# Optimization experiments

Measured on AMD Instinct MI355X. Metric: run time of the kernel, lower is better.

The kernel has to match this reference:

```python
import jax, jax.numpy as jnp
import numpy as np

NUM_EMBEDDINGS = 1024
EMBEDDING_SIZE = 256


def setup_inputs() -> dict:
    key = jax.random.key(0)
    k1, k2 = jax.random.split(key)
    z_e = jax.random.normal(k1, (32, 32, 32, EMBEDDING_SIZE), dtype=jnp.float32)
    # original init: uniform(-limit, limit), limit = sqrt(3/num_embeddings)
    limit = np.sqrt(3.0 / NUM_EMBEDDINGS)
    embeddings = jax.random.uniform(
        k2, (NUM_EMBEDDINGS, EMBEDDING_SIZE), dtype=jnp.float32,
        minval=-limit, maxval=limit)
    return {"z_e": z_e, "embeddings": embeddings}


def reference(z_e, embeddings):
    D = embeddings.shape[1]
    z_e_flat = z_e.reshape(-1, D)  # [N, D]
    distances = (
        jnp.sum(z_e_flat * z_e_flat, axis=1, keepdims=True)
        - 2.0 * (z_e_flat @ embeddings.T)
        + jnp.sum(embeddings * embeddings, axis=1)[None, :]
    )  # [N, K]
    z = jnp.argmin(distances, axis=-1).reshape(z_e.shape[:-1])  # indices
    z_q = embeddings[z]  # gather -> same shape as z_e
    return z, z_q
```

## Files before the change

kernel.cpp:

```cpp
#include <hip/hip_runtime.h>
#include <math.h>

#define N_ROWS 32768
#define DIM 256
#define K_CODES 1024
#define MARGIN 2e-3f

typedef float f32x4v __attribute__((ext_vector_type(4)));
typedef short s16x8 __attribute__((ext_vector_type(8)));

#define WS_NEEDED ((size_t)1183748)

__device__ __forceinline__ unsigned short bf16_rne(float f) {
    unsigned int u = __float_as_uint(f);
    unsigned int r = (u + 0x7FFFu + ((u >> 16) & 1u)) >> 16;
    return (unsigned short)r;
}
__device__ __forceinline__ float bf16_f32(unsigned short h) {
    return __uint_as_float(((unsigned int)h) << 16);
}

__device__ __forceinline__ float np_block128_sumsq(const float* e) {
#pragma clang fp contract(off)
    float s[16];
#pragma unroll
    for (int l = 0; l < 16; ++l) {
        float a0 = e[l]       * e[l];
        float a1 = e[16 + l]  * e[16 + l];
        float a2 = e[32 + l]  * e[32 + l];
        float a3 = e[48 + l]  * e[48 + l];
        float a4 = e[64 + l]  * e[64 + l];
        float a5 = e[80 + l]  * e[80 + l];
        float a6 = e[96 + l]  * e[96 + l];
        float a7 = e[112 + l] * e[112 + l];
        s[l] = ((a0 + a1) + (a2 + a3)) + ((a4 + a5) + (a6 + a7));
    }
    float t1[8];
#pragma unroll
    for (int i = 0; i < 8; ++i) t1[i] = s[i] + s[i + 8];
    float t2[4];
#pragma unroll
    for (int i = 0; i < 4; ++i) t2[i] = t1[i] + t1[i + 4];
    return (t2[0] + t2[2]) + (t2[1] + t2[3]);
}

__global__ __launch_bounds__(64) void npsumsq_kernel(const float* __restrict__ src,
                                                     float* __restrict__ dst) {
    __shared__ float buf[16][257];
    const int tid = threadIdx.x;
    const int r0 = blockIdx.x * 16;
#pragma unroll
    for (int it = 0; it < 16; ++it) {
        int idx = it * 64 + tid;
        int r = idx >> 6, c4 = idx & 63;
        float4 v = ((const float4*)(src + (size_t)(r0 + r) * DIM))[c4];
        buf[r][c4 * 4 + 0] = v.x;
        buf[r][c4 * 4 + 1] = v.y;
        buf[r][c4 * 4 + 2] = v.z;
        buf[r][c4 * 4 + 3] = v.w;
    }
    __syncthreads();
    if (tid < 16) {
        const float* e = buf[tid];
        dst[r0 + tid] = np_block128_sumsq(e) + np_block128_sumsq(e + 128);
    }
}

__global__ void zero_kernel(int* p) { if (threadIdx.x == 0) p[0] = 0; }

__global__ __launch_bounds__(64) void wprep_kernel(const float* __restrict__ w,
                                                   float* __restrict__ w2,
                                                   unsigned short* __restrict__ wfrag) {
    __shared__ float buf[16][257];
    const int lane = threadIdx.x;
    const int t = blockIdx.x;
    const int r0 = t * 16;
#pragma unroll
    for (int it = 0; it < 16; ++it) {
        int idx = it * 64 + lane;
        int r = idx >> 6, c4 = idx & 63;
        float4 v = ((const float4*)(w + (size_t)(r0 + r) * DIM))[c4];
        buf[r][c4 * 4 + 0] = v.x;
        buf[r][c4 * 4 + 1] = v.y;
        buf[r][c4 * 4 + 2] = v.z;
        buf[r][c4 * 4 + 3] = v.w;
    }
    __syncthreads();
    if (lane < 16) {
        const float* e = buf[lane];
        w2[r0 + lane] = np_block128_sumsq(e) + np_block128_sumsq(e + 128);
    }
    const int c = lane & 15, ko = lane >> 4;
#pragma unroll
    for (int q = 0; q < 8; ++q) {
        s16x8 hh, ll;
#pragma unroll
        for (int i = 0; i < 8; ++i) {
            float f = buf[c][q * 32 + ko * 8 + i];
            unsigned short h = bf16_rne(f);
            hh[i] = (short)h;
            ll[i] = (short)bf16_rne(f - bf16_f32(h));
        }
        unsigned short* dh = wfrag + (size_t)t * 8192 + q * 512 + lane * 8;
        *(s16x8*)dh = hh;
        *(s16x8*)(dh + 4096) = ll;
    }
}

__global__ __launch_bounds__(256, 1) void vq_mfma(
    const float* __restrict__ x, const uint4* __restrict__ wfrag4,
    const float* __restrict__ w2g, const float* __restrict__ w,
    float* __restrict__ zout, float* __restrict__ zq,
    int* __restrict__ flagcnt, int* __restrict__ flaglist) {
    __shared__ uint4 tiles[2][1024];
    __shared__ float sw2[K_CODES];
    __shared__ int widx_s[128];

    const int tid = threadIdx.x;
    const int wave = tid >> 6;
    const int lane = tid & 63;
    const int rowblk = blockIdx.x * 128;
    const int rowbase = rowblk + wave * 32;

    for (int i = tid; i < K_CODES; i += 256) sw2[i] = w2g[i];

    s16x8 ahi0[8], alo0[8], ahi1[8], alo1[8];
    {
        const float* xr0 = x + (size_t)(rowbase + (lane & 15)) * DIM + (lane >> 4) * 8;
        const float* xr1 = xr0 + 16 * DIM;
#pragma unroll
        for (int q = 0; q < 8; ++q) {
            float4 a = *(const float4*)(xr0 + q * 32);
            float4 b = *(const float4*)(xr0 + q * 32 + 4);
            float e0[8] = {a.x, a.y, a.z, a.w, b.x, b.y, b.z, b.w};
            float4 c = *(const float4*)(xr1 + q * 32);
            float4 d = *(const float4*)(xr1 + q * 32 + 4);
            float e1[8] = {c.x, c.y, c.z, c.w, d.x, d.y, d.z, d.w};
#pragma unroll
            for (int i = 0; i < 8; ++i) {
                unsigned short h0 = bf16_rne(e0[i]);
                ahi0[q][i] = (short)h0;
                alo0[q][i] = (short)bf16_rne(e0[i] - bf16_f32(h0));
                unsigned short h1 = bf16_rne(e1[i]);
                ahi1[q][i] = (short)h1;
                alo1[q][i] = (short)bf16_rne(e1[i] - bf16_f32(h1));
            }
        }
    }

#pragma unroll
    for (int s = 0; s < 4; ++s) {
        int idx = wave * 256 + s * 64 + lane;
        tiles[0][idx] = wfrag4[idx];
    }

    float b1[2][4], b2[2][4];
    int i1[2][4];
#pragma unroll
    for (int rf = 0; rf < 2; ++rf)
#pragma unroll
        for (int j = 0; j < 4; ++j) { b1[rf][j] = INFINITY; b2[rf][j] = INFINITY; i1[rf][j] = 0; }

    __syncthreads();

    int cur = 0;
    for (int ct = 0; ct < 64; ++ct) {
        uint4 pf0, pf1, pf2, pf3;
        if (ct < 63) {
            const uint4* g = wfrag4 + (size_t)(ct + 1) * 1024 + wave * 256 + lane;
            pf0 = g[0]; pf1 = g[64]; pf2 = g[128]; pf3 = g[192];
        }
        const uint4* th = tiles[cur];
        f32x4v a0hh = {0.f, 0.f, 0.f, 0.f};
        f32x4v a0hl = {0.f, 0.f, 0.f, 0.f};
        f32x4v a0lh = {0.f, 0.f, 0.f, 0.f};
        f32x4v a1hh = {0.f, 0.f, 0.f, 0.f};
        f32x4v a1hl = {0.f, 0.f, 0.f, 0.f};
        f32x4v a1lh = {0.f, 0.f, 0.f, 0.f};
#pragma unroll
        for (int q = 0; q < 8; ++q) {
            s16x8 Bh = *(const s16x8*)&th[q * 64 + lane];
            s16x8 Bl = *(const s16x8*)&th[512 + q * 64 + lane];
            a0hh = __builtin_amdgcn_mfma_f32_16x16x32_bf16(ahi0[q], Bh, a0hh, 0, 0, 0);
            a0hl = __builtin_amdgcn_mfma_f32_16x16x32_bf16(ahi0[q], Bl, a0hl, 0, 0, 0);
            a0lh = __builtin_amdgcn_mfma_f32_16x16x32_bf16(alo0[q], Bh, a0lh, 0, 0, 0);
            a1hh = __builtin_amdgcn_mfma_f32_16x16x32_bf16(ahi1[q], Bh, a1hh, 0, 0, 0);
            a1hl = __builtin_amdgcn_mfma_f32_16x16x32_bf16(ahi1[q], Bl, a1hl, 0, 0, 0);
            a1lh = __builtin_amdgcn_mfma_f32_16x16x32_bf16(alo1[q], Bh, a1lh, 0, 0, 0);
        }
        const int code = ct * 16 + (lane & 15);
        const float w2v = sw2[code];
#pragma unroll
        for (int j = 0; j < 4; ++j) {
            float d0 = (a0hh[j] + a0hl[j]) + a0lh[j];
            float s0 = w2v - 2.0f * d0;
            if (s0 < b2[0][j]) {
                if (s0 < b1[0][j]) { b2[0][j] = b1[0][j]; b1[0][j] = s0; i1[0][j] = code; }
                else b2[0][j] = s0;
            }
            float d1 = (a1hh[j] + a1hl[j]) + a1lh[j];
            float s1 = w2v - 2.0f * d1;
            if (s1 < b2[1][j]) {
                if (s1 < b1[1][j]) { b2[1][j] = b1[1][j]; b1[1][j] = s1; i1[1][j] = code; }
                else b2[1][j] = s1;
            }
        }
        if (ct < 63) {
            uint4* d = &tiles[cur ^ 1][wave * 256 + lane];
            d[0] = pf0; d[64] = pf1; d[128] = pf2; d[192] = pf3;
            cur ^= 1;
        }
        __syncthreads();
    }

#pragma unroll
    for (int m = 1; m < 16; m <<= 1) {
#pragma unroll
        for (int rf = 0; rf < 2; ++rf)
#pragma unroll
            for (int j = 0; j < 4; ++j) {
                float ov1 = __shfl_xor(b1[rf][j], m);
                int oi = __shfl_xor(i1[rf][j], m);
                float ov2 = __shfl_xor(b2[rf][j], m);
                float nb2 = fminf(fmaxf(b1[rf][j], ov1), fminf(b2[rf][j], ov2));
                if (ov1 < b1[rf][j] || (ov1 == b1[rf][j] && oi < i1[rf][j])) {
                    b1[rf][j] = ov1; i1[rf][j] = oi;
                }
                b2[rf][j] = nb2;
            }
    }
    if ((lane & 15) == 0) {
#pragma unroll
        for (int rf = 0; rf < 2; ++rf)
#pragma unroll
            for (int j = 0; j < 4; ++j) {
                int rl = wave * 32 + rf * 16 + (lane >> 4) * 4 + j;
                int gi = i1[rf][j];
                widx_s[rl] = gi;
                zout[rowblk + rl] = (float)gi;
                if (b2[rf][j] - b1[rf][j] < MARGIN) {
                    int slot = atomicAdd(flagcnt, 1);
                    flaglist[slot] = rowblk + rl;
                }
            }
    }
    __syncthreads();

    const float4* w4 = (const float4*)w;
    float4* zq4 = (float4*)zq;
#pragma unroll
    for (int p = 0; p < 32; ++p) {
        int lin = p * 256 + tid;
        int row = lin >> 6, qq = lin & 63;
        zq4[(size_t)(rowblk + row) * 64 + qq] = w4[(size_t)widx_s[row] * 64 + qq];
    }
}

__global__ __launch_bounds__(256) void rescue_kernel(
    const float* __restrict__ x, const float* __restrict__ w,
    const float* __restrict__ w2g, const int* __restrict__ flagcnt,
    const int* __restrict__ flaglist, float* __restrict__ zout,
    float* __restrict__ zq) {
    __shared__ __align__(16) float xs[DIM];
    __shared__ float dv[256];
    __shared__ int di[256];
    __shared__ int mi_s;
    __shared__ float x2_s;
    const int tid = threadIdx.x;
    const int cnt = flagcnt[0];
    for (int f = blockIdx.x; f < cnt; f += gridDim.x) {
        const int r = flaglist[f];
        __syncthreads();
        for (int i = tid; i < DIM; i += 256) xs[i] = x[(size_t)r * DIM + i];
        __syncthreads();
        if (tid == 0)
            x2_s = np_block128_sumsq(xs) + np_block128_sumsq(xs + 128);
        __syncthreads();
        const float x2vv = x2_s;
        const float4* xs4 = (const float4*)xs;
        const float4* wr0 = (const float4*)(w + (size_t)(tid + 0 * 256) * DIM);
        const float4* wr1 = (const float4*)(w + (size_t)(tid + 1 * 256) * DIM);
        const float4* wr2 = (const float4*)(w + (size_t)(tid + 2 * 256) * DIM);
        const float4* wr3 = (const float4*)(w + (size_t)(tid + 3 * 256) * DIM);
        float acc0 = 0.f, acc1 = 0.f, acc2 = 0.f, acc3 = 0.f;
#pragma unroll 4
        for (int k4 = 0; k4 < DIM / 4; ++k4) {
            float4 xv = xs4[k4];
            float4 w0 = wr0[k4], w1 = wr1[k4], w2 = wr2[k4], w3 = wr3[k4];
            acc0 = __builtin_fmaf(xv.x, w0.x, acc0);
            acc0 = __builtin_fmaf(xv.y, w0.y, acc0);
            acc0 = __builtin_fmaf(xv.z, w0.z, acc0);
            acc0 = __builtin_fmaf(xv.w, w0.w, acc0);
            acc1 = __builtin_fmaf(xv.x, w1.x, acc1);
            acc1 = __builtin_fmaf(xv.y, w1.y, acc1);
            acc1 = __builtin_fmaf(xv.z, w1.z, acc1);
            acc1 = __builtin_fmaf(xv.w, w1.w, acc1);
            acc2 = __builtin_fmaf(xv.x, w2.x, acc2);
            acc2 = __builtin_fmaf(xv.y, w2.y, acc2);
            acc2 = __builtin_fmaf(xv.z, w2.z, acc2);
            acc2 = __builtin_fmaf(xv.w, w2.w, acc2);
            acc3 = __builtin_fmaf(xv.x, w3.x, acc3);
            acc3 = __builtin_fmaf(xv.y, w3.y, acc3);
            acc3 = __builtin_fmaf(xv.z, w3.z, acc3);
            acc3 = __builtin_fmaf(xv.w, w3.w, acc3);
        }
        float bv = INFINITY;
        int bi = 0;
        float accs[4] = {acc0, acc1, acc2, acc3};
#pragma unroll
        for (int cc = 0; cc < 4; ++cc) {
            int c = tid + cc * 256;
            float s = (x2vv - 2.0f * accs[cc]) + w2g[c];
            if (s < bv) { bv = s; bi = c; }
        }
        dv[tid] = bv;
        di[tid] = bi;
        __syncthreads();
        if (tid == 0) {
            float mv = dv[0];
            int mi = di[0];
            for (int t = 1; t < 256; ++t)
                if (dv[t] < mv || (dv[t] == mv && di[t] < mi)) { mv = dv[t]; mi = di[t]; }
            zout[r] = (float)mi;
            mi_s = mi;
        }
        __syncthreads();
        zq[(size_t)r * DIM + tid] = w[(size_t)mi_s * DIM + tid];
    }
}

#define BM 64
#define BN 128
#define BK 64
#define LDX 68

__global__ __launch_bounds__(256) void vq_kernel_lds(
    const float* __restrict__ x, const float* __restrict__ w,
    const float* __restrict__ x2g, const float* __restrict__ w2g,
    float* __restrict__ zout, float* __restrict__ zq) {
    __shared__ float xs[BM * LDX];
    __shared__ float ws_[BN * LDX];
    __shared__ float sw2[K_CODES];
    __shared__ float sx2[BM];
    __shared__ int widx[BM];

    const int tid = threadIdx.x;
    const int bm0 = blockIdx.x * BM;
    const int rg = tid & 15;
    const int cg = tid >> 4;

    for (int i = tid; i < K_CODES; i += 256) sw2[i] = w2g[i];
    if (tid < BM) sx2[tid] = x2g[bm0 + tid];

    float best[4];
    int bidx[4];
#pragma unroll
    for (int i = 0; i < 4; ++i) { best[i] = INFINITY; bidx[i] = 0; }

    const float4* x4 = (const float4*)x;
    const float4* w4 = (const float4*)w;

    for (int cn = 0; cn < K_CODES / BN; ++cn) {
        float acc[4][8];
#pragma unroll
        for (int i = 0; i < 4; ++i)
#pragma unroll
            for (int j = 0; j < 8; ++j) acc[i][j] = 0.f;

        for (int dk = 0; dk < DIM / BK; ++dk) {
            __syncthreads();
#pragma unroll
            for (int p = 0; p < 4; ++p) {
                int l = p * 256 + tid;
                int row = l >> 4, c4 = l & 15;
                float4 v = x4[(size_t)(bm0 + row) * (DIM / 4) + dk * (BK / 4) + c4];
                *(float4*)&xs[row * LDX + c4 * 4] = v;
            }
#pragma unroll
            for (int p = 0; p < 8; ++p) {
                int l = p * 256 + tid;
                int row = l >> 4, c4 = l & 15;
                float4 v = w4[(size_t)(cn * BN + row) * (DIM / 4) + dk * (BK / 4) + c4];
                *(float4*)&ws_[row * LDX + c4 * 4] = v;
            }
            __syncthreads();
#pragma unroll
            for (int d = 0; d < BK; d += 4) {
                float4 xv[4], wv[8];
#pragma unroll
                for (int i = 0; i < 4; ++i)
                    xv[i] = *(const float4*)&xs[(rg + 16 * i) * LDX + d];
#pragma unroll
                for (int j = 0; j < 8; ++j)
                    wv[j] = *(const float4*)&ws_[(cg + 16 * j) * LDX + d];
#pragma unroll
                for (int i = 0; i < 4; ++i)
#pragma unroll
                    for (int j = 0; j < 8; ++j) {
                        acc[i][j] = __builtin_fmaf(xv[i].x, wv[j].x, acc[i][j]);
                        acc[i][j] = __builtin_fmaf(xv[i].y, wv[j].y, acc[i][j]);
                        acc[i][j] = __builtin_fmaf(xv[i].z, wv[j].z, acc[i][j]);
                        acc[i][j] = __builtin_fmaf(xv[i].w, wv[j].w, acc[i][j]);
                    }
            }
        }
#pragma unroll
        for (int j = 0; j < 8; ++j) {
            int c = cn * BN + cg + 16 * j;
            float w2v = sw2[c];
#pragma unroll
            for (int i = 0; i < 4; ++i) {
                float t = sx2[rg + 16 * i] - 2.0f * acc[i][j];
                float s = t + w2v;
                if (s < best[i]) { best[i] = s; bidx[i] = c; }
            }
        }
    }

    __syncthreads();
    float* sval = xs;
    int* sidx = (int*)(xs + 64 * 17);
#pragma unroll
    for (int i = 0; i < 4; ++i) {
        sval[(rg + 16 * i) * 17 + cg] = best[i];
        sidx[(rg + 16 * i) * 17 + cg] = bidx[i];
    }
    __syncthreads();
    if (tid < BM) {
        float bv = INFINITY;
        int bi = 0;
        for (int c = 0; c < 16; ++c) {
            float v = sval[tid * 17 + c];
            int id = sidx[tid * 17 + c];
            if (v < bv || (v == bv && id < bi)) { bv = v; bi = id; }
        }
        widx[tid] = bi;
        zout[bm0 + tid] = (float)bi;
    }
    __syncthreads();
    float4* zq4 = (float4*)zq;
#pragma unroll
    for (int p = 0; p < 16; ++p) {
        int lin = p * 256 + tid;
        int row = lin >> 6, q = lin & 63;
        zq4[(size_t)(bm0 + row) * 64 + q] = w4[(size_t)widx[row] * 64 + q];
    }
}

extern "C" void kernel_launch(void* const* d_in, const int* in_sizes, int n_in,
                              void* d_out, int out_size, void* d_ws, size_t ws_size,
                              hipStream_t stream) {
    const float* z_e = (const float*)d_in[0];
    const float* emb = (const float*)d_in[1];
    float* x2g = (float*)d_ws;
    int* flaglist = (int*)d_ws;
    float* w2g = x2g + N_ROWS;
    unsigned short* wfrag = (unsigned short*)(w2g + K_CODES);
    int* flagcnt = (int*)(wfrag + (size_t)2 * K_CODES * DIM);
    float* zout = (float*)d_out;
    float* zq = (float*)d_out + N_ROWS;

    if (ws_size >= WS_NEEDED) {
        zero_kernel<<<1, 64, 0, stream>>>(flagcnt);
        wprep_kernel<<<K_CODES / 16, 64, 0, stream>>>(emb, w2g, wfrag);
        vq_mfma<<<N_ROWS / 128, 256, 0, stream>>>(z_e, (const uint4*)wfrag, w2g,
                                                  emb, zout, zq, flagcnt, flaglist);
        rescue_kernel<<<256, 256, 0, stream>>>(z_e, emb, w2g, flagcnt,
                                               flaglist, zout, zq);
    } else {
        npsumsq_kernel<<<N_ROWS / 16, 64, 0, stream>>>(z_e, x2g);
        npsumsq_kernel<<<K_CODES / 16, 64, 0, stream>>>(emb, w2g);
        vq_kernel_lds<<<N_ROWS / BM, 256, 0, stream>>>(z_e, emb, x2g, w2g, zout, zq);
    }
}
```

Measured before the change: 150.6 us.

## Split VQ MFMA block into eight waves of 16 rows each

Each 128-row block now runs 512 threads (8 waves) with 16 rows per wave, where it used to run 4 waves with 32 rows each. Every wave holds half as many A fragments and accumulators, and tile loading and the gather are spread over twice as many threads. The goal is more wave-level parallelism per CU to hide LDS and MFMA latency. The cost is that B-tile reads from LDS are amortised over fewer rows per wave, so LDS traffic per MFMA doubles.

```diff
diff --git a/kernel.cpp b/kernel.cpp
--- a/kernel.cpp
+++ b/kernel.cpp
@@ -107,7 +107,7 @@
     }
 }
 
-__global__ __launch_bounds__(256, 1) void vq_mfma(
+__global__ __launch_bounds__(512, 1) void vq_mfma(
     const float* __restrict__ x, const uint4* __restrict__ wfrag4,
     const float* __restrict__ w2g, const float* __restrict__ w,
     float* __restrict__ zout, float* __restrict__ zq,
@@ -120,94 +120,72 @@
     const int wave = tid >> 6;
     const int lane = tid & 63;
     const int rowblk = blockIdx.x * 128;
-    const int rowbase = rowblk + wave * 32;
-
-    for (int i = tid; i < K_CODES; i += 256) sw2[i] = w2g[i];
-
-    s16x8 ahi0[8], alo0[8], ahi1[8], alo1[8];
+    const int rowbase = rowblk + wave * 16;
+
+    for (int i = tid; i < K_CODES; i += 512) sw2[i] = w2g[i];
+
+    s16x8 ahi[8], alo[8];
     {
-        const float* xr0 = x + (size_t)(rowbase + (lane & 15)) * DIM + (lane >> 4) * 8;
-        const float* xr1 = xr0 + 16 * DIM;
+        const float* xr = x + (size_t)(rowbase + (lane & 15)) * DIM + (lane >> 4) * 8;
 #pragma unroll
         for (int q = 0; q < 8; ++q) {
-            float4 a = *(const float4*)(xr0 + q * 32);
-            float4 b = *(const float4*)(xr0 + q * 32 + 4);
-            float e0[8] = {a.x, a.y, a.z, a.w, b.x, b.y, b.z, b.w};
-            float4 c = *(const float4*)(xr1 + q * 32);
-            float4 d = *(const float4*)(xr1 + q * 32 + 4);
-            float e1[8] = {c.x, c.y, c.z, c.w, d.x, d.y, d.z, d.w};
+            float4 a = *(const float4*)(xr + q * 32);
+            float4 b = *(const float4*)(xr + q * 32 + 4);
+            float e[8] = {a.x, a.y, a.z, a.w, b.x, b.y, b.z, b.w};
 #pragma unroll
             for (int i = 0; i < 8; ++i) {
-                unsigned short h0 = bf16_rne(e0[i]);
-                ahi0[q][i] = (short)h0;
-                alo0[q][i] = (short)bf16_rne(e0[i] - bf16_f32(h0));
-                unsigned short h1 = bf16_rne(e1[i]);
-                ahi1[q][i] = (short)h1;
-                alo1[q][i] = (short)bf16_rne(e1[i] - bf16_f32(h1));
-            }
-        }
-    }
-
-#pragma unroll
-    for (int s = 0; s < 4; ++s) {
-        int idx = wave * 256 + s * 64 + lane;
-        tiles[0][idx] = wfrag4[idx];
-    }
-
-    float b1[2][4], b2[2][4];
-    int i1[2][4];
-#pragma unroll
-    for (int rf = 0; rf < 2; ++rf)
-#pragma unroll
-        for (int j = 0; j < 4; ++j) { b1[rf][j] = INFINITY; b2[rf][j] = INFINITY; i1[rf][j] = 0; }
+                unsigned short h = bf16_rne(e[i]);
+                ahi[q][i] = (short)h;
+                alo[q][i] = (short)bf16_rne(e[i] - bf16_f32(h));
+            }
+        }
+    }
+
+    tiles[0][tid] = wfrag4[tid];
+    tiles[0][tid + 512] = wfrag4[tid + 512];
+
+    float b1[4], b2[4];
+    int i1[4];
+#pragma unroll
+    for (int j = 0; j < 4; ++j) { b1[j] = INFINITY; b2[j] = INFINITY; i1[j] = 0; }
 
     __syncthreads();
 
     int cur = 0;
     for (int ct = 0; ct < 64; ++ct) {
-        uint4 pf0, pf1, pf2, pf3;
+        uint4 pf0, pf1;
         if (ct < 63) {
-            const uint4* g = wfrag4 + (size_t)(ct + 1) * 1024 + wave * 256 + lane;
-            pf0 = g[0]; pf1 = g[64]; pf2 = g[128]; pf3 = g[192];
+            const uint4* g = wfrag4 + (size_t)(ct + 1) * 1024;
+            pf0 = g[tid];
+            pf1 = g[tid + 512];
         }
         const uint4* th = tiles[cur];
-        f32x4v a0hh = {0.f, 0.f, 0.f, 0.f};
-        f32x4v a0hl = {0.f, 0.f, 0.f, 0.f};
-        f32x4v a0lh = {0.f, 0.f, 0.f, 0.f};
-        f32x4v a1hh = {0.f, 0.f, 0.f, 0.f};
-        f32x4v a1hl = {0.f, 0.f, 0.f, 0.f};
-        f32x4v a1lh = {0.f, 0.f, 0.f, 0.f};
+        f32x4v ahh = {0.f, 0.f, 0.f, 0.f};
+        f32x4v ahl = {0.f, 0.f, 0.f, 0.f};
+        f32x4v alh = {0.f, 0.f, 0.f, 0.f};
 #pragma unroll
         for (int q = 0; q < 8; ++q) {
             s16x8 Bh = *(const s16x8*)&th[q * 64 + lane];
             s16x8 Bl = *(const s16x8*)&th[512 + q * 64 + lane];
-            a0hh = __builtin_amdgcn_mfma_f32_16x16x32_bf16(ahi0[q], Bh, a0hh, 0, 0, 0);
-            a0hl = __builtin_amdgcn_mfma_f32_16x16x32_bf16(ahi0[q], Bl, a0hl, 0, 0, 0);
-            a0lh = __builtin_amdgcn_mfma_f32_16x16x32_bf16(alo0[q], Bh, a0lh, 0, 0, 0);
-            a1hh = __builtin_amdgcn_mfma_f32_16x16x32_bf16(ahi1[q], Bh, a1hh, 0, 0, 0);
-            a1hl = __builtin_amdgcn_mfma_f32_16x16x32_bf16(ahi1[q], Bl, a1hl, 0, 0, 0);
-            a1lh = __builtin_amdgcn_mfma_f32_16x16x32_bf16(alo1[q], Bh, a1lh, 0, 0, 0);
+            ahh = __builtin_amdgcn_mfma_f32_16x16x32_bf16(ahi[q], Bh, ahh, 0, 0, 0);
+            ahl = __builtin_amdgcn_mfma_f32_16x16x32_bf16(ahi[q], Bl, ahl, 0, 0, 0);
+            alh = __builtin_amdgcn_mfma_f32_16x16x32_bf16(alo[q], Bh, alh, 0, 0, 0);
         }
         const int code = ct * 16 + (lane & 15);
         const float w2v = sw2[code];
 #pragma unroll
         for (int j = 0; j < 4; ++j) {
-            float d0 = (a0hh[j] + a0hl[j]) + a0lh[j];
-            float s0 = w2v - 2.0f * d0;
-            if (s0 < b2[0][j]) {
-                if (s0 < b1[0][j]) { b2[0][j] = b1[0][j]; b1[0][j] = s0; i1[0][j] = code; }
-                else b2[0][j] = s0;
-            }
-            float d1 = (a1hh[j] + a1hl[j]) + a1lh[j];
-            float s1 = w2v - 2.0f * d1;
-            if (s1 < b2[1][j]) {
-                if (s1 < b1[1][j]) { b2[1][j] = b1[1][j]; b1[1][j] = s1; i1[1][j] = code; }
-                else b2[1][j] = s1;
+            float d = (ahh[j] + ahl[j]) + alh[j];
+            float s = w2v - 2.0f * d;
+            if (s < b2[j]) {
+                if (s < b1[j]) { b2[j] = b1[j]; b1[j] = s; i1[j] = code; }
+                else b2[j] = s;
             }
         }
         if (ct < 63) {
-            uint4* d = &tiles[cur ^ 1][wave * 256 + lane];
-            d[0] = pf0; d[64] = pf1; d[128] = pf2; d[192] = pf3;
+            uint4* d = tiles[cur ^ 1];
+            d[tid] = pf0;
+            d[tid + 512] = pf1;
             cur ^= 1;
         }
         __syncthreads();
@@ -216,41 +194,34 @@
 #pragma unroll
     for (int m = 1; m < 16; m <<= 1) {
 #pragma unroll
-        for (int rf = 0; rf < 2; ++rf)
-#pragma unroll
-            for (int j = 0; j < 4; ++j) {
-                float ov1 = __shfl_xor(b1[rf][j], m);
-                int oi = __shfl_xor(i1[rf][j], m);
-                float ov2 = __shfl_xor(b2[rf][j], m);
-                float nb2 = fminf(fmaxf(b1[rf][j], ov1), fminf(b2[rf][j], ov2));
-                if (ov1 < b1[rf][j] || (ov1 == b1[rf][j] && oi < i1[rf][j])) {
-                    b1[rf][j] = ov1; i1[rf][j] = oi;
-                }
-                b2[rf][j] = nb2;
-            }
+        for (int j = 0; j < 4; ++j) {
+            float ov1 = __shfl_xor(b1[j], m);
+            int oi = __shfl_xor(i1[j], m);
+            float ov2 = __shfl_xor(b2[j], m);
+            float nb2 = fminf(fmaxf(b1[j], ov1), fminf(b2[j], ov2));
+            if (ov1 < b1[j] || (ov1 == b1[j] && oi < i1[j])) { b1[j] = ov1; i1[j] = oi; }
+            b2[j] = nb2;
+        }
     }
     if ((lane & 15) == 0) {
 #pragma unroll
-        for (int rf = 0; rf < 2; ++rf)
-#pragma unroll
-            for (int j = 0; j < 4; ++j) {
-                int rl = wave * 32 + rf * 16 + (lane >> 4) * 4 + j;
-                int gi = i1[rf][j];
-                widx_s[rl] = gi;
-                zout[rowblk + rl] = (float)gi;
-                if (b2[rf][j] - b1[rf][j] < MARGIN) {
-                    int slot = atomicAdd(flagcnt, 1);
-                    flaglist[slot] = rowblk + rl;
-                }
-            }
+        for (int j = 0; j < 4; ++j) {
+            int rl = wave * 16 + (lane >> 4) * 4 + j;
+            widx_s[rl] = i1[j];
+            zout[rowblk + rl] = (float)i1[j];
+            if (b2[j] - b1[j] < MARGIN) {
+                int slot = atomicAdd(flagcnt, 1);
+                flaglist[slot] = rowblk + rl;
+            }
+        }
     }
     __syncthreads();
 
     const float4* w4 = (const float4*)w;
     float4* zq4 = (float4*)zq;
 #pragma unroll
-    for (int p = 0; p < 32; ++p) {
-        int lin = p * 256 + tid;
+    for (int p = 0; p < 16; ++p) {
+        int lin = p * 512 + tid;
         int row = lin >> 6, qq = lin & 63;
         zq4[(size_t)(rowblk + row) * 64 + qq] = w4[(size_t)widx_s[row] * 64 + qq];
     }
@@ -463,7 +434,7 @@
     if (ws_size >= WS_NEEDED) {
         zero_kernel<<<1, 64, 0, stream>>>(flagcnt);
         wprep_kernel<<<K_CODES / 16, 64, 0, stream>>>(emb, w2g, wfrag);
-        vq_mfma<<<N_ROWS / 128, 256, 0, stream>>>(z_e, (const uint4*)wfrag, w2g,
+        vq_mfma<<<N_ROWS / 128, 512, 0, stream>>>(z_e, (const uint4*)wfrag, w2g,
                                                   emb, zout, zq, flagcnt, flaglist);
         rescue_kernel<<<256, 256, 0, stream>>>(z_e, emb, w2g, flagcnt,
                                                flaglist, zout, zq);
```

New measurement: 136.1 us. -9.6%, faster.

## Split codebook scan across two wave groups per block and drop zero kernel

Applied to the files above, without the earlier changes.

The MFMA kernel now runs 512 threads per block. Two groups of four waves each scan alternating 16-code tiles for the same 128 rows, and their top-2 results are merged through shared memory at the end. This halves the serial loop length per wave and raises occupancy to two blocks per CU. The cost is duplicated A-fragment registers and a larger LDS tile buffer. The separate zero_kernel launch is folded into wprep_kernel to save one launch.

```diff
diff --git a/kernel.cpp b/kernel.cpp
--- a/kernel.cpp
+++ b/kernel.cpp
@@ -66,15 +66,15 @@
     }
 }
 
-__global__ void zero_kernel(int* p) { if (threadIdx.x == 0) p[0] = 0; }
-
 __global__ __launch_bounds__(64) void wprep_kernel(const float* __restrict__ w,
                                                    float* __restrict__ w2,
-                                                   unsigned short* __restrict__ wfrag) {
+                                                   unsigned short* __restrict__ wfrag,
+                                                   int* __restrict__ flagcnt) {
     __shared__ float buf[16][257];
     const int lane = threadIdx.x;
     const int t = blockIdx.x;
     const int r0 = t * 16;
+    if (t == 0 && lane == 0) flagcnt[0] = 0;
 #pragma unroll
     for (int it = 0; it < 16; ++it) {
         int idx = it * 64 + lane;
@@ -107,22 +107,26 @@
     }
 }
 
-__global__ __launch_bounds__(256, 1) void vq_mfma(
+__global__ __launch_bounds__(512, 2) void vq_mfma(
     const float* __restrict__ x, const uint4* __restrict__ wfrag4,
     const float* __restrict__ w2g, const float* __restrict__ w,
     float* __restrict__ zout, float* __restrict__ zq,
     int* __restrict__ flagcnt, int* __restrict__ flaglist) {
-    __shared__ uint4 tiles[2][1024];
+    __shared__ uint4 tiles[2][2048];
     __shared__ float sw2[K_CODES];
+    __shared__ float M1[128], M2[128];
+    __shared__ int MI[128];
     __shared__ int widx_s[128];
 
     const int tid = threadIdx.x;
     const int wave = tid >> 6;
     const int lane = tid & 63;
+    const int wg = wave >> 2;
+    const int wsub = wave & 3;
     const int rowblk = blockIdx.x * 128;
-    const int rowbase = rowblk + wave * 32;
-
-    for (int i = tid; i < K_CODES; i += 256) sw2[i] = w2g[i];
+    const int rowbase = rowblk + wsub * 32;
+
+    for (int i = tid; i < K_CODES; i += 512) sw2[i] = w2g[i];
 
     s16x8 ahi0[8], alo0[8], ahi1[8], alo1[8];
     {
@@ -148,11 +152,10 @@
         }
     }
 
-#pragma unroll
-    for (int s = 0; s < 4; ++s) {
-        int idx = wave * 256 + s * 64 + lane;
-        tiles[0][idx] = wfrag4[idx];
-    }
+    tiles[0][tid] = wfrag4[tid];
+    tiles[0][tid + 512] = wfrag4[tid + 512];
+    tiles[0][tid + 1024] = wfrag4[tid + 1024];
+    tiles[0][tid + 1536] = wfrag4[tid + 1536];
 
     float b1[2][4], b2[2][4];
     int i1[2][4];
@@ -164,13 +167,14 @@
     __syncthreads();
 
     int cur = 0;
-    for (int ct = 0; ct < 64; ++ct) {
+    for (int p = 0; p < 32; ++p) {
         uint4 pf0, pf1, pf2, pf3;
-        if (ct < 63) {
-            const uint4* g = wfrag4 + (size_t)(ct + 1) * 1024 + wave * 256 + lane;
-            pf0 = g[0]; pf1 = g[64]; pf2 = g[128]; pf3 = g[192];
-        }
-        const uint4* th = tiles[cur];
+        if (p < 31) {
+            const uint4* g = wfrag4 + (size_t)(2 * p + 2) * 1024;
+            pf0 = g[tid]; pf1 = g[tid + 512];
+            pf2 = g[tid + 1024]; pf3 = g[tid + 1536];
+        }
+        const uint4* th = &tiles[cur][wg * 1024];
         f32x4v a0hh = {0.f, 0.f, 0.f, 0.f};
         f32x4v a0hl = {0.f, 0.f, 0.f, 0.f};
         f32x4v a0lh = {0.f, 0.f, 0.f, 0.f};
@@ -188,7 +192,7 @@
             a1hl = __builtin_amdgcn_mfma_f32_16x16x32_bf16(ahi1[q], Bl, a1hl, 0, 0, 0);
             a1lh = __builtin_amdgcn_mfma_f32_16x16x32_bf16(alo1[q], Bh, a1lh, 0, 0, 0);
         }
-        const int code = ct * 16 + (lane & 15);
+        const int code = (2 * p + wg) * 16 + (lane & 15);
         const float w2v = sw2[code];
 #pragma unroll
         for (int j = 0; j < 4; ++j) {
@@ -205,9 +209,10 @@
                 else b2[1][j] = s1;
             }
         }
-        if (ct < 63) {
-            uint4* d = &tiles[cur ^ 1][wave * 256 + lane];
-            d[0] = pf0; d[64] = pf1; d[128] = pf2; d[192] = pf3;
+        if (p < 31) {
+            uint4* d = tiles[cur ^ 1];
+            d[tid] = pf0; d[tid + 512] = pf1;
+            d[tid + 1024] = pf2; d[tid + 1536] = pf3;
             cur ^= 1;
         }
         __syncthreads();
@@ -229,16 +234,36 @@
                 b2[rf][j] = nb2;
             }
     }
-    if ((lane & 15) == 0) {
+    if (wg == 1 && (lane & 15) == 0) {
 #pragma unroll
         for (int rf = 0; rf < 2; ++rf)
 #pragma unroll
             for (int j = 0; j < 4; ++j) {
-                int rl = wave * 32 + rf * 16 + (lane >> 4) * 4 + j;
-                int gi = i1[rf][j];
+                int rl = wsub * 32 + rf * 16 + (lane >> 4) * 4 + j;
+                M1[rl] = b1[rf][j];
+                M2[rl] = b2[rf][j];
+                MI[rl] = i1[rf][j];
+            }
+    }
+    __syncthreads();
+    if (wg == 0 && (lane & 15) == 0) {
+#pragma unroll
+        for (int rf = 0; rf < 2; ++rf)
+#pragma unroll
+            for (int j = 0; j < 4; ++j) {
+                int rl = wsub * 32 + rf * 16 + (lane >> 4) * 4 + j;
+                float a1 = b1[rf][j], a2 = b2[rf][j];
+                int ai = i1[rf][j];
+                float o1 = M1[rl], o2 = M2[rl];
+                int oi = MI[rl];
+                float g1;
+                int gi;
+                if (o1 < a1 || (o1 == a1 && oi < ai)) { g1 = o1; gi = oi; }
+                else { g1 = a1; gi = ai; }
+                float g2 = fminf(fmaxf(a1, o1), fminf(a2, o2));
                 widx_s[rl] = gi;
                 zout[rowblk + rl] = (float)gi;
-                if (b2[rf][j] - b1[rf][j] < MARGIN) {
+                if (g2 - g1 < MARGIN) {
                     int slot = atomicAdd(flagcnt, 1);
                     flaglist[slot] = rowblk + rl;
                 }
@@ -249,8 +274,8 @@
     const float4* w4 = (const float4*)w;
     float4* zq4 = (float4*)zq;
 #pragma unroll
-    for (int p = 0; p < 32; ++p) {
-        int lin = p * 256 + tid;
+    for (int p2 = 0; p2 < 16; ++p2) {
+        int lin = p2 * 512 + tid;
         int row = lin >> 6, qq = lin & 63;
         zq4[(size_t)(rowblk + row) * 64 + qq] = w4[(size_t)widx_s[row] * 64 + qq];
     }
@@ -461,9 +486,8 @@
     float* zq = (float*)d_out + N_ROWS;
 
     if (ws_size >= WS_NEEDED) {
-        zero_kernel<<<1, 64, 0, stream>>>(flagcnt);
-        wprep_kernel<<<K_CODES / 16, 64, 0, stream>>>(emb, w2g, wfrag);
-        vq_mfma<<<N_ROWS / 128, 256, 0, stream>>>(z_e, (const uint4*)wfrag, w2g,
+        wprep_kernel<<<K_CODES / 16, 64, 0, stream>>>(emb, w2g, wfrag, flagcnt);
+        vq_mfma<<<N_ROWS / 128, 512, 0, stream>>>(z_e, (const uint4*)wfrag, w2g,
                                                   emb, zout, zq, flagcnt, flaglist);
         rescue_kernel<<<256, 256, 0, stream>>>(z_e, emb, w2g, flagcnt,
                                                flaglist, zout, zq);
```

New measurement: 142.0 us. 1.06x faster.
